# Optimization experiments

Hardware: AMD Instinct MI355X
Metric: run time of the kernel (lower is better)

The kernel has to match this reference:

```python
import jax, jax.numpy as jnp
import numpy as np

B, C, H, W = 2, 512, 64, 64
GROUPS = 32
EPS = 1e-6


def setup_inputs() -> dict:
    key = jax.random.key(0)
    ks = jax.random.split(key, 9)
    s = 1.0 / np.sqrt(C)
    return {
        "x": jax.random.normal(ks[0], (B, C, H, W), dtype=jnp.float32),
        "gamma": jnp.ones((C,), dtype=jnp.float32),
        "beta": jnp.zeros((C,), dtype=jnp.float32),
        "wq": jax.random.normal(ks[1], (C, C), dtype=jnp.float32) * s,
        "bq": jnp.zeros((C,), dtype=jnp.float32),
        "wk": jax.random.normal(ks[2], (C, C), dtype=jnp.float32) * s,
        "bk": jnp.zeros((C,), dtype=jnp.float32),
        "wv": jax.random.normal(ks[3], (C, C), dtype=jnp.float32) * s,
        "bv": jnp.zeros((C,), dtype=jnp.float32),
        "wp": jax.random.normal(ks[4], (C, C), dtype=jnp.float32) * s,
        "bp": jnp.zeros((C,), dtype=jnp.float32),
    }


def _group_norm(x, gamma, beta):
    b, c, h, w = x.shape
    xg = x.reshape(b, GROUPS, c // GROUPS, h, w)
    mean = jnp.mean(xg, axis=(2, 3, 4), keepdims=True)
    var = jnp.var(xg, axis=(2, 3, 4), keepdims=True)
    xn = ((xg - mean) * jax.lax.rsqrt(var + EPS)).reshape(b, c, h, w)
    return xn * gamma[None, :, None, None] + beta[None, :, None, None]


def reference(x, gamma, beta, wq, bq, wk, bk, wv, bv, wp, bp):
    b, c, h, w = x.shape
    hn = _group_norm(x, gamma, beta)
    # 1x1 convs == per-pixel linear; flatten spatial: (b, hw, c)
    t = hn.reshape(b, c, h * w).transpose(0, 2, 1)
    q = jnp.einsum('bnc,oc->bno', t, wq) + bq
    k = jnp.einsum('bnc,oc->bno', t, wk) + bk
    v = jnp.einsum('bnc,oc->bno', t, wv) + bv
    scale = float(int(c) ** (-0.5))
    attn = jax.nn.softmax(jnp.einsum('bic,bjc->bij', q, k) * scale, axis=-1)
    o = jnp.einsum('bij,bjc->bic', attn, v)  # (b, hw, c)
    o = jnp.einsum('bnc,oc->bno', o, wp) + bp
    o = o.transpose(0, 2, 1).reshape(b, c, h, w)
    return x + o
```

## Files before the change

kernel.cpp:

```cpp
#include <hip/hip_runtime.h>
#include <hip/hip_bf16.h>

#define B_ 2
#define C_ 512
#define HW_ 4096
#define K_ 512
#define EPS_ 1e-6f
#define SCALE_ 0.04419417382415922f
#define NEG_INF_ (-1e30f)

typedef __attribute__((ext_vector_type(8))) __bf16 bf16x8;
typedef __attribute__((ext_vector_type(4))) float f32x4;
typedef __attribute__((ext_vector_type(16))) float f32x16;

__device__ __forceinline__ unsigned short f2bf(float f) {
  union { float f; unsigned u; } v; v.f = f;
  unsigned r = v.u + 0x7fffu + ((v.u >> 16) & 1u);
  return (unsigned short)(r >> 16);
}
__device__ __forceinline__ float bf2f(unsigned short h) {
  union { unsigned u; float f; } v; v.u = ((unsigned)h) << 16;
  return v.f;
}

__device__ __forceinline__ void gld_lds16(const unsigned short* g, unsigned short* l) {
  __builtin_amdgcn_global_load_lds((const __attribute__((address_space(1))) void*)g,
                                   (__attribute__((address_space(3))) void*)l, 16, 0, 0);
}

__global__ void gn_sums(const float* __restrict__ x, float* __restrict__ stats) {
  int bid = blockIdx.x;
  int bg = bid >> 4, row = bid & 15;
  int b = bg >> 5, g = bg & 31;
  const float* base = x + ((size_t)(b * C_ + g * 16 + row)) * HW_;
  float s = 0.f, s2 = 0.f;
  int t = threadIdx.x;
  #pragma unroll
  for (int i = 0; i < 4; ++i) {
    float4 v = *reinterpret_cast<const float4*>(base + (size_t)(t + i * 256) * 4);
    s  += v.x + v.y + v.z + v.w;
    s2 += v.x * v.x + v.y * v.y + v.z * v.z + v.w * v.w;
  }
  for (int off = 32; off; off >>= 1) { s += __shfl_down(s, off); s2 += __shfl_down(s2, off); }
  __shared__ float rs[4], rs2[4];
  int w = t >> 6;
  if ((t & 63) == 0) { rs[w] = s; rs2[w] = s2; }
  __syncthreads();
  if (t == 0) {
    atomicAdd(&stats[bg], rs[0] + rs[1] + rs[2] + rs[3]);
    atomicAdd(&stats[64 + bg], rs2[0] + rs2[1] + rs2[2] + rs2[3]);
  }
}

__global__ void build_t(const float* __restrict__ x, const float* __restrict__ stats,
                        const float* __restrict__ gamma, const float* __restrict__ beta,
                        unsigned short* __restrict__ tb) {
  __shared__ float lds[64 * 69];
  int n0 = blockIdx.x * 64, c0 = blockIdx.y * 64, b = blockIdx.z;
  int t = threadIdx.x;
  {
    int cl = t >> 2, ch = t & 3;
    int c = c0 + cl;
    int bg = b * 32 + (c >> 4);
    float s = stats[bg], s2v = stats[64 + bg];
    float mean = s * (1.f / 65536.f);
    float var = s2v * (1.f / 65536.f) - mean * mean;
    float rstd = rsqrtf(var + EPS_);
    float ga = gamma[c] * rstd;
    float be = beta[c] - mean * ga;
    const float* xr = x + ((size_t)(b * C_ + c)) * HW_ + n0 + ch * 16;
    #pragma unroll
    for (int i = 0; i < 4; ++i) {
      float4 v = *reinterpret_cast<const float4*>(xr + i * 4);
      int nl = ch * 16 + i * 4;
      lds[cl * 69 + nl + 0] = v.x * ga + be;
      lds[cl * 69 + nl + 1] = v.y * ga + be;
      lds[cl * 69 + nl + 2] = v.z * ga + be;
      lds[cl * 69 + nl + 3] = v.w * ga + be;
    }
  }
  __syncthreads();
  {
    int nl = t >> 2, cw = t & 3;
    unsigned short* orow = tb + ((size_t)(b * HW_ + n0 + nl)) * C_ + c0 + cw * 16;
    #pragma unroll
    for (int i = 0; i < 4; ++i) {
      ushort4 o4;
      o4.x = f2bf(lds[(cw * 16 + i * 4 + 0) * 69 + nl]);
      o4.y = f2bf(lds[(cw * 16 + i * 4 + 1) * 69 + nl]);
      o4.z = f2bf(lds[(cw * 16 + i * 4 + 2) * 69 + nl]);
      o4.w = f2bf(lds[(cw * 16 + i * 4 + 3) * 69 + nl]);
      *reinterpret_cast<ushort4*>(orow + i * 4) = o4;
    }
  }
}

__global__ void cast_w4(const float* __restrict__ s0, const float* __restrict__ s1,
                        const float* __restrict__ s2, const float* __restrict__ s3,
                        unsigned short* __restrict__ dst) {
  int which = blockIdx.y;
  const float* src = which == 0 ? s0 : which == 1 ? s1 : which == 2 ? s2 : s3;
  int i = (blockIdx.x * 256 + threadIdx.x) * 4;
  float4 v = *reinterpret_cast<const float4*>(src + i);
  ushort4 o; o.x = f2bf(v.x); o.y = f2bf(v.y); o.z = f2bf(v.z); o.w = f2bf(v.w);
  *reinterpret_cast<ushort4*>(dst + (size_t)which * 262144 + i) = o;
}

__global__ __launch_bounds__(256, 2) void gemm_qkv(
    const unsigned short* __restrict__ tb, const unsigned short* __restrict__ wqkv,
    const float* __restrict__ bq, const float* __restrict__ bk, const float* __restrict__ bv,
    unsigned short* __restrict__ qb, unsigned short* __restrict__ kb,
    unsigned short* __restrict__ vTb) {
  __shared__ unsigned short Al[2][128 * 64];
  __shared__ unsigned short Bl[2][128 * 64];
  int z = blockIdx.z;
  int which = z >> 1, b = z & 1;
  const unsigned short* Ab = (which < 2) ? (tb + (size_t)b * HW_ * K_) : (wqkv + 2 * 262144);
  const unsigned short* Bb = (which < 2) ? (wqkv + which * 262144) : (tb + (size_t)b * HW_ * K_);
  int m0 = (which < 2) ? blockIdx.y * 128 : blockIdx.x * 128;
  int n0 = (which < 2) ? blockIdx.x * 128 : blockIdx.y * 128;
  int N = (which < 2) ? 512 : HW_;
  unsigned short* Cb = (which == 0) ? (qb + (size_t)b * HW_ * K_)
                     : (which == 1) ? (kb + (size_t)b * HW_ * K_)
                                    : (vTb + (size_t)b * C_ * HW_);
  const float* bias = (which == 0) ? bq : (which == 1) ? bk : bv;
  int t = threadIdx.x, lane = t & 63, w = t >> 6;
  int l15 = lane & 15, quad = lane >> 4;
  int mw = (w & 1) * 64, nw = (w >> 1) * 64;
  int sr8 = lane >> 3, sb = lane & 7;
  f32x4 acc[4][4] = {};

  #define G_STAGE(KC) do {                                                          \
    int pb = (KC) & 1;                                                              \
    _Pragma("unroll")                                                               \
    for (int q = 0; q < 4; ++q) {                                                   \
      int row = w * 32 + q * 8 + sr8;                                               \
      int gb = sb ^ (row & 7);                                                      \
      gld_lds16(Ab + (size_t)(m0 + row) * K_ + (KC) * 64 + gb * 8, &Al[pb][(w * 32 + q * 8) * 64]); \
      gld_lds16(Bb + (size_t)(n0 + row) * K_ + (KC) * 64 + gb * 8, &Bl[pb][(w * 32 + q * 8) * 64]); \
    }                                                                               \
  } while (0)

  G_STAGE(0);
  __syncthreads();
  for (int kc = 0; kc < 8; ++kc) {
    if (kc < 7) G_STAGE(kc + 1);
    const unsigned short* Ac = Al[kc & 1];
    const unsigned short* Bc = Bl[kc & 1];
    #pragma unroll
    for (int kk = 0; kk < 2; ++kk) {
      bf16x8 af[4];
      #pragma unroll
      for (int mt = 0; mt < 4; ++mt)
        af[mt] = *reinterpret_cast<const bf16x8*>(
            &Ac[(mw + mt * 16 + l15) * 64 + (((kk * 4 + quad) ^ (l15 & 7)) << 3)]);
      #pragma unroll
      for (int nt = 0; nt < 4; ++nt) {
        bf16x8 bfr = *reinterpret_cast<const bf16x8*>(
            &Bc[(nw + nt * 16 + l15) * 64 + (((kk * 4 + quad) ^ (l15 & 7)) << 3)]);
        #pragma unroll
        for (int mt = 0; mt < 4; ++mt)
          acc[mt][nt] = __builtin_amdgcn_mfma_f32_16x16x32_bf16(af[mt], bfr, acc[mt][nt], 0, 0, 0);
      }
    }
    __syncthreads();
  }
  #undef G_STAGE
  #pragma unroll
  for (int mt = 0; mt < 4; ++mt)
    #pragma unroll
    for (int nt = 0; nt < 4; ++nt)
      #pragma unroll
      for (int rr = 0; rr < 4; ++rr) {
        int row = m0 + mw + mt * 16 + quad * 4 + rr;
        int col = n0 + nw + nt * 16 + l15;
        float v = acc[mt][nt][rr] + ((which < 2) ? bias[col] : bias[row]);
        Cb[(size_t)row * N + col] = f2bf(v);
      }
}

template <int MODE>
__global__ __launch_bounds__(256, 2) void gemm_bt(
    const unsigned short* __restrict__ A, long sA,
    const unsigned short* __restrict__ B, long sB,
    void* __restrict__ Cv, long sC, int M, int N,
    const float* __restrict__ bias,
    const float* __restrict__ resid, long sR) {
  __shared__ unsigned short Al[2][128 * 64];
  __shared__ unsigned short Bl[2][128 * 64];
  int z = blockIdx.z;
  const unsigned short* Ab = A + (size_t)z * sA;
  const unsigned short* Bb = B + (size_t)z * sB;
  int n0 = blockIdx.x * 128, m0 = blockIdx.y * 128;
  int t = threadIdx.x, lane = t & 63, w = t >> 6;
  int l15 = lane & 15, quad = lane >> 4;
  int mw = (w & 1) * 64, nw = (w >> 1) * 64;
  int sr8 = lane >> 3, sb = lane & 7;
  f32x4 acc[4][4] = {};

  #define G_STAGE(KC) do {                                                          \
    int pb = (KC) & 1;                                                              \
    _Pragma("unroll")                                                               \
    for (int q = 0; q < 4; ++q) {                                                   \
      int row = w * 32 + q * 8 + sr8;                                               \
      int gb = sb ^ (row & 7);                                                      \
      gld_lds16(Ab + (size_t)(m0 + row) * K_ + (KC) * 64 + gb * 8, &Al[pb][(w * 32 + q * 8) * 64]); \
      gld_lds16(Bb + (size_t)(n0 + row) * K_ + (KC) * 64 + gb * 8, &Bl[pb][(w * 32 + q * 8) * 64]); \
    }                                                                               \
  } while (0)

  G_STAGE(0);
  __syncthreads();
  for (int kc = 0; kc < 8; ++kc) {
    if (kc < 7) G_STAGE(kc + 1);
    const unsigned short* Ac = Al[kc & 1];
    const unsigned short* Bc = Bl[kc & 1];
    #pragma unroll
    for (int kk = 0; kk < 2; ++kk) {
      bf16x8 af[4];
      #pragma unroll
      for (int mt = 0; mt < 4; ++mt)
        af[mt] = *reinterpret_cast<const bf16x8*>(
            &Ac[(mw + mt * 16 + l15) * 64 + (((kk * 4 + quad) ^ (l15 & 7)) << 3)]);
      #pragma unroll
      for (int nt = 0; nt < 4; ++nt) {
        bf16x8 bfr = *reinterpret_cast<const bf16x8*>(
            &Bc[(nw + nt * 16 + l15) * 64 + (((kk * 4 + quad) ^ (l15 & 7)) << 3)]);
        #pragma unroll
        for (int mt = 0; mt < 4; ++mt)
          acc[mt][nt] = __builtin_amdgcn_mfma_f32_16x16x32_bf16(af[mt], bfr, acc[mt][nt], 0, 0, 0);
      }
    }
    __syncthreads();
  }
  #undef G_STAGE
  #pragma unroll
  for (int mt = 0; mt < 4; ++mt)
    #pragma unroll
    for (int nt = 0; nt < 4; ++nt)
      #pragma unroll
      for (int rr = 0; rr < 4; ++rr) {
        int row = m0 + mw + mt * 16 + quad * 4 + rr;
        int col = n0 + nw + nt * 16 + l15;
        float v = acc[mt][nt][rr];
        if (MODE == 0) {
          v += bias[col];
          reinterpret_cast<unsigned short*>(Cv)[(size_t)z * sC + (size_t)row * N + col] = f2bf(v);
        } else if (MODE == 1) {
          v += bias[row];
          reinterpret_cast<unsigned short*>(Cv)[(size_t)z * sC + (size_t)row * N + col] = f2bf(v);
        } else {
          v += bias[row];
          v += resid[(size_t)z * sR + (size_t)row * N + col];
          reinterpret_cast<float*>(Cv)[(size_t)z * sC + (size_t)row * N + col] = v;
        }
      }
}

__global__ __launch_bounds__(512, 2) void attn(
    const unsigned short* __restrict__ qg, const unsigned short* __restrict__ kg,
    const unsigned short* __restrict__ vg,
    unsigned short* __restrict__ opart, float* __restrict__ mpart, float* __restrict__ lpart) {
  __shared__ unsigned short KVb[2 * 16384];
  __shared__ unsigned short Pl[64 * 264];
  __shared__ float sm_m[64], sm_l[64], sm_alpha[64], sm_red[128];
  int qt = blockIdx.x, jh = blockIdx.y, b = blockIdx.z;
  int t = threadIdx.x, lane = t & 63, w = t >> 6;
  int l15 = lane & 15, quad = lane >> 4;
  int l31 = lane & 31, hl = lane >> 5;
  int rw = w & 3, cw = w >> 2;
  int rw2 = w & 1, dg = w >> 1;
  int m0 = qt * 64;
  if (t < 64) { sm_m[t] = NEG_INF_; sm_l[t] = 0.f; }

  int st_r[4], st_kb[4];
  #pragma unroll
  for (int q = 0; q < 4; ++q) {
    int blk = w * 4 + q;
    st_r[q] = blk * 4 + (lane >> 4);
    st_kb[q] = (lane & 15) ^ (st_r[q] & 7);
  }

  #define STAGE_K(JC, KC, J0) do {                                                  \
    const unsigned short* gb = kg + ((size_t)(b * HW_ + (J0) + (JC) * 128)) * K_ + (KC) * 128; \
    unsigned short* lb = KVb + ((((JC) * 4 + (KC)) & 1) << 14);                     \
    _Pragma("unroll")                                                               \
    for (int q = 0; q < 4; ++q)                                                     \
      gld_lds16(gb + (size_t)st_r[q] * K_ + st_kb[q] * 8, lb + (w * 4 + q) * 512);  \
  } while (0)

  #define STAGE_V(DC, JC, J0) do {                                                 \
    const unsigned short* gb = vg + ((size_t)(b * K_ + (DC) * 128)) * HW_ + (J0) + (JC) * 128; \
    unsigned short* lb = KVb + (((DC) & 1) << 14);                                  \
    _Pragma("unroll")                                                               \
    for (int q = 0; q < 4; ++q)                                                     \
      gld_lds16(gb + (size_t)st_r[q] * HW_ + st_kb[q] * 8, lb + (w * 4 + q) * 512); \
  } while (0)

  bf16x8 qa[16];
  {
    const unsigned short* qrow = qg + ((size_t)(b * HW_ + m0 + rw * 16 + l15)) * K_ + quad * 8;
    #pragma unroll
    for (int kk = 0; kk < 16; ++kk)
      qa[kk] = *reinterpret_cast<const bf16x8*>(qrow + kk * 32);
  }
  f32x16 acc_o[4] = {};

  int j0 = jh * 2048;
  STAGE_K(0, 0, j0);
  __syncthreads();

  for (int it = 0; it < 8; ++it, j0 += 256) {
    f32x4 acc_s[8] = {};
    #pragma unroll
    for (int c = 0; c < 8; ++c) {
      int jc = c >> 2, kc = c & 3;
      if (c < 7) { STAGE_K((c + 1) >> 2, (c + 1) & 3, j0); }
      else       { STAGE_V(0, 0, j0); }
      const unsigned short* bufc = KVb + ((c & 1) << 14);
      #pragma unroll
      for (int kk = 0; kk < 4; ++kk)
        #pragma unroll
        for (int ct = 0; ct < 4; ++ct) {
          int jr = cw * 64 + ct * 16 + l15;
          bf16x8 bfr = *reinterpret_cast<const bf16x8*>(
              &bufc[jr * 128 + (((kk * 4 + quad) ^ (l15 & 7)) << 3)]);
          acc_s[jc * 4 + ct] = __builtin_amdgcn_mfma_f32_16x16x32_bf16(qa[kc * 4 + kk], bfr, acc_s[jc * 4 + ct], 0, 0, 0);
        }
      __syncthreads();
    }
    float mx[4];
    #pragma unroll
    for (int rr = 0; rr < 4; ++rr) {
      float m = NEG_INF_;
      #pragma unroll
      for (int s = 0; s < 8; ++s) {
        acc_s[s][rr] *= SCALE_;
        m = fmaxf(m, acc_s[s][rr]);
      }
      mx[rr] = m;
    }
    #pragma unroll
    for (int off = 1; off < 16; off <<= 1)
      #pragma unroll
      for (int rr = 0; rr < 4; ++rr)
        mx[rr] = fmaxf(mx[rr], __shfl_xor(mx[rr], off));
    if (l15 == 0)
      #pragma unroll
      for (int rr = 0; rr < 4; ++rr)
        sm_red[cw * 64 + rw * 16 + quad * 4 + rr] = mx[rr];
    __syncthreads();
    if (t < 64) {
      float mnew = fmaxf(sm_m[t], fmaxf(sm_red[t], sm_red[64 + t]));
      sm_alpha[t] = __expf(sm_m[t] - mnew);
      sm_m[t] = mnew;
    }
    __syncthreads();
    float sum[4] = {0.f, 0.f, 0.f, 0.f};
    #pragma unroll
    for (int s = 0; s < 8; ++s)
      #pragma unroll
      for (int rr = 0; rr < 4; ++rr) {
        int rowl = rw * 16 + quad * 4 + rr;
        float p = __expf(acc_s[s][rr] - sm_m[rowl]);
        sum[rr] += p;
        Pl[rowl * 264 + (s >> 2) * 128 + cw * 64 + (s & 3) * 16 + l15] = f2bf(p);
      }
    #pragma unroll
    for (int off = 1; off < 16; off <<= 1)
      #pragma unroll
      for (int rr = 0; rr < 4; ++rr)
        sum[rr] += __shfl_xor(sum[rr], off);
    if (l15 == 0)
      #pragma unroll
      for (int rr = 0; rr < 4; ++rr)
        sm_red[cw * 64 + rw * 16 + quad * 4 + rr] = sum[rr];
    __syncthreads();
    if (t < 64)
      sm_l[t] = sm_l[t] * sm_alpha[t] + sm_red[t] + sm_red[64 + t];
    #pragma unroll
    for (int r16 = 0; r16 < 16; ++r16) {
      int row = rw2 * 32 + (r16 & 3) + 8 * (r16 >> 2) + 4 * hl;
      float a = sm_alpha[row];
      #pragma unroll
      for (int dc = 0; dc < 4; ++dc)
        acc_o[dc][r16] *= a;
    }
    bf16x8 pa_r[8];
    #pragma unroll
    for (int c = 0; c < 8; ++c) {
      int jc = c >> 2, dc = c & 3;
      if ((c & 3) == 0) {
        #pragma unroll
        for (int ksx = 0; ksx < 8; ++ksx)
          pa_r[ksx] = *reinterpret_cast<const bf16x8*>(
              &Pl[(rw2 * 32 + l31) * 264 + jc * 128 + ksx * 16 + hl * 8]);
      }
      if (c < 7)          { STAGE_V((c + 1) & 3, (c + 1) >> 2, j0); }
      else if (it < 7)    { STAGE_K(0, 0, j0 + 256); }
      const unsigned short* bufc = KVb + ((c & 1) << 14);
      #pragma unroll
      for (int ksx = 0; ksx < 8; ++ksx) {
        bf16x8 vb = *reinterpret_cast<const bf16x8*>(
            &bufc[(dg * 32 + l31) * 128 + (((ksx * 2 + hl) ^ (l31 & 7)) << 3)]);
        acc_o[dc] = __builtin_amdgcn_mfma_f32_32x32x16_bf16(pa_r[ksx], vb, acc_o[dc], 0, 0, 0);
      }
      __syncthreads();
    }
  }
  #undef STAGE_K
  #undef STAGE_V
  int part = jh * 2 + b;
  unsigned short* ob = opart + ((size_t)part * HW_ + m0) * 512;
  #pragma unroll
  for (int dc = 0; dc < 4; ++dc) {
    int d = dc * 128 + dg * 32 + l31;
    #pragma unroll
    for (int r16 = 0; r16 < 16; ++r16) {
      int row = rw2 * 32 + (r16 & 3) + 8 * (r16 >> 2) + 4 * hl;
      ob[(size_t)row * 512 + d] = f2bf(acc_o[dc][r16]);
    }
  }
  if (t < 64) {
    mpart[(size_t)part * HW_ + m0 + t] = sm_m[t];
    lpart[(size_t)part * HW_ + m0 + t] = sm_l[t];
  }
}

__global__ void merge_o(const unsigned short* __restrict__ opart, const float* __restrict__ mpart,
                        const float* __restrict__ lpart, unsigned short* __restrict__ om) {
  int rg = blockIdx.x;
  int b = rg >> 12, n = rg & 4095;
  float m[2], l[2], M = NEG_INF_;
  #pragma unroll
  for (int p = 0; p < 2; ++p) {
    size_t r = (size_t)(p * 2 + b) * HW_ + n;
    m[p] = mpart[r]; l[p] = lpart[r];
    M = fmaxf(M, m[p]);
  }
  float wgt[2], L = 0.f;
  #pragma unroll
  for (int p = 0; p < 2; ++p) { wgt[p] = __expf(m[p] - M); L += l[p] * wgt[p]; }
  float inv = 1.f / L;
  unsigned short* orow = om + (size_t)rg * 512;
  for (int d = threadIdx.x; d < 512; d += 256) {
    float acc = 0.f;
    #pragma unroll
    for (int p = 0; p < 2; ++p)
      acc += bf2f(opart[((size_t)(p * 2 + b) * HW_ + n) * 512 + d]) * wgt[p];
    orow[d] = f2bf(acc * inv);
  }
}

extern "C" void kernel_launch(void* const* d_in, const int* in_sizes, int n_in,
                              void* d_out, int out_size, void* d_ws, size_t ws_size,
                              hipStream_t stream) {
  const float* x     = (const float*)d_in[0];
  const float* gamma = (const float*)d_in[1];
  const float* beta  = (const float*)d_in[2];
  const float* wq    = (const float*)d_in[3];
  const float* bq    = (const float*)d_in[4];
  const float* wk    = (const float*)d_in[5];
  const float* bk    = (const float*)d_in[6];
  const float* wv    = (const float*)d_in[7];
  const float* bv    = (const float*)d_in[8];
  const float* wp    = (const float*)d_in[9];
  const float* bp    = (const float*)d_in[10];
  float* out = (float*)d_out;

  char* ws = (char*)d_ws;
  size_t o = 0;
  float* stats          = (float*)(ws + o);          o += 1024;
  unsigned short* tb    = (unsigned short*)(ws + o); o += 8388608;
  unsigned short* qb    = (unsigned short*)(ws + o); o += 8388608;
  unsigned short* kb    = (unsigned short*)(ws + o); o += 8388608;
  unsigned short* vTb   = (unsigned short*)(ws + o); o += 8388608;
  unsigned short* wqb   = (unsigned short*)(ws + o); o += 524288;
  unsigned short* wkb   = (unsigned short*)(ws + o); o += 524288;
  unsigned short* wvb   = (unsigned short*)(ws + o); o += 524288;
  unsigned short* wpb   = (unsigned short*)(ws + o); o += 524288;
  unsigned short* opart = (unsigned short*)(ws + o); o += 16777216;
  float* mpart          = (float*)(ws + o);          o += 65536;
  float* lpart          = (float*)(ws + o);          o += 65536;
  unsigned short* om    = tb;

  hipMemsetAsync(stats, 0, 512, stream);
  gn_sums<<<1024, 256, 0, stream>>>(x, stats);
  build_t<<<dim3(64, 8, 2), 256, 0, stream>>>(x, stats, gamma, beta, tb);
  cast_w4<<<dim3(256, 4), 256, 0, stream>>>(wq, wk, wv, wp, wqb);
  gemm_qkv<<<dim3(4, 32, 6), 256, 0, stream>>>(tb, wqb, bq, bk, bv, qb, kb, vTb);
  attn<<<dim3(64, 2, 2), 512, 0, stream>>>(qb, kb, vTb, opart, mpart, lpart);
  merge_o<<<8192, 256, 0, stream>>>(opart, mpart, lpart, om);
  gemm_bt<2><<<dim3(32, 4, 2), 256, 0, stream>>>(wpb, 0, om, (long)HW_ * K_, out, (long)C_ * HW_, C_, HW_, bp, x, (long)C_ * HW_);
}
```

Before: 279.6 us.

## Triple-buffer K/V staging in attention with vmcnt-based waits and priority hints

The attention kernel's K/V LDS staging moves from two buffers to three, with loads issued two chunks ahead. The full __syncthreads calls are replaced by raw s_barrier plus an explicit vmcnt wait, so global-to-LDS copies stay in flight across MFMA phases. s_setprio is raised around MFMA blocks, and the softmax reduction barriers become lgkmcnt-only waits. merge_o is also vectorized to handle two bf16 values per thread. The larger LDS footprint may reduce occupancy, and the hand-tuned waitcnt and barrier logic risks races.

```diff
diff --git a/kernel.cpp b/kernel.cpp
--- a/kernel.cpp
+++ b/kernel.cpp
@@ -261,7 +261,7 @@
     const unsigned short* __restrict__ qg, const unsigned short* __restrict__ kg,
     const unsigned short* __restrict__ vg,
     unsigned short* __restrict__ opart, float* __restrict__ mpart, float* __restrict__ lpart) {
-  __shared__ unsigned short KVb[2 * 16384];
+  __shared__ unsigned short KVb[3 * 16384];
   __shared__ unsigned short Pl[64 * 264];
   __shared__ float sm_m[64], sm_l[64], sm_alpha[64], sm_red[128];
   int qt = blockIdx.x, jh = blockIdx.y, b = blockIdx.z;
@@ -281,20 +281,38 @@
     st_kb[q] = (lane & 15) ^ (st_r[q] & 7);
   }
 
-  #define STAGE_K(JC, KC, J0) do {                                                  \
-    const unsigned short* gb = kg + ((size_t)(b * HW_ + (J0) + (JC) * 128)) * K_ + (KC) * 128; \
-    unsigned short* lb = KVb + ((((JC) * 4 + (KC)) & 1) << 14);                     \
-    _Pragma("unroll")                                                               \
-    for (int q = 0; q < 4; ++q)                                                     \
-      gld_lds16(gb + (size_t)st_r[q] * K_ + st_kb[q] * 8, lb + (w * 4 + q) * 512);  \
+  #define STAGE_CH(Q, J0V, LB) do {                                                 \
+    if ((Q) < 8) {                                                                  \
+      const unsigned short* gb = kg + ((size_t)(b * HW_ + (J0V) + ((Q) >> 2) * 128)) * K_ + ((Q) & 3) * 128; \
+      _Pragma("unroll")                                                             \
+      for (int q_ = 0; q_ < 4; ++q_)                                                \
+        gld_lds16(gb + (size_t)st_r[q_] * K_ + st_kb[q_] * 8, (LB) + (w * 4 + q_) * 512); \
+    } else if ((Q) < 16) {                                                          \
+      const unsigned short* gb = vg + ((size_t)(b * K_ + (((Q) - 8) & 3) * 128)) * HW_ + (J0V) + (((Q) - 8) >> 2) * 128; \
+      _Pragma("unroll")                                                             \
+      for (int q_ = 0; q_ < 4; ++q_)                                                \
+        gld_lds16(gb + (size_t)st_r[q_] * HW_ + st_kb[q_] * 8, (LB) + (w * 4 + q_) * 512); \
+    } else {                                                                        \
+       \
+      const unsigned short* gb = kg + ((size_t)(b * HW_ + (J0V) + 256)) * K_ + ((Q) - 16) * 128; \
+      _Pragma("unroll")                                                             \
+      for (int q_ = 0; q_ < 4; ++q_)                                                \
+        gld_lds16(gb + (size_t)st_r[q_] * K_ + st_kb[q_] * 8, (LB) + (w * 4 + q_) * 512); \
+    }                                                                               \
   } while (0)
 
-  #define STAGE_V(DC, JC, J0) do {                                                 \
-    const unsigned short* gb = vg + ((size_t)(b * K_ + (DC) * 128)) * HW_ + (J0) + (JC) * 128; \
-    unsigned short* lb = KVb + (((DC) & 1) << 14);                                  \
-    _Pragma("unroll")                                                               \
-    for (int q = 0; q < 4; ++q)                                                     \
-      gld_lds16(gb + (size_t)st_r[q] * HW_ + st_kb[q] * 8, lb + (w * 4 + q) * 512); \
+  #define PHASE_PRE(Q) do {                                                         \
+    __builtin_amdgcn_s_barrier();                 \
+    int bs_ = bufr + 2; if (bs_ >= 3) bs_ -= 3;                                     \
+    STAGE_CH(Q, j0, KVb + bs_ * 16384);                                             \
+    asm volatile("s_waitcnt vmcnt(8)" ::: "memory");     \
+    __builtin_amdgcn_s_barrier();                  \
+    __builtin_amdgcn_sched_barrier(0);                                              \
+  } while (0)
+  #define PHASE_POST() do { bufr = (bufr + 1 >= 3) ? 0 : bufr + 1; } while (0)
+  #define LGKM_BAR() do {                                                           \
+    asm volatile("s_waitcnt lgkmcnt(0)" ::: "memory");                              \
+    __builtin_amdgcn_s_barrier();                                                   \
   } while (0)
 
   bf16x8 qa[16];
@@ -307,17 +325,18 @@
   f32x16 acc_o[4] = {};
 
   int j0 = jh * 2048;
-  STAGE_K(0, 0, j0);
-  __syncthreads();
+  int bufr = 0;
+  STAGE_CH(0, j0, KVb + 0 * 16384);
+  STAGE_CH(1, j0, KVb + 1 * 16384);
 
   for (int it = 0; it < 8; ++it, j0 += 256) {
     f32x4 acc_s[8] = {};
     #pragma unroll
     for (int c = 0; c < 8; ++c) {
-      int jc = c >> 2, kc = c & 3;
-      if (c < 7) { STAGE_K((c + 1) >> 2, (c + 1) & 3, j0); }
-      else       { STAGE_V(0, 0, j0); }
-      const unsigned short* bufc = KVb + ((c & 1) << 14);
+      PHASE_PRE(c + 2);
+      const unsigned short* bufc = KVb + bufr * 16384;
+      int jc = c >> 2;
+      __builtin_amdgcn_s_setprio(1);
       #pragma unroll
       for (int kk = 0; kk < 4; ++kk)
         #pragma unroll
@@ -325,9 +344,10 @@
           int jr = cw * 64 + ct * 16 + l15;
           bf16x8 bfr = *reinterpret_cast<const bf16x8*>(
               &bufc[jr * 128 + (((kk * 4 + quad) ^ (l15 & 7)) << 3)]);
-          acc_s[jc * 4 + ct] = __builtin_amdgcn_mfma_f32_16x16x32_bf16(qa[kc * 4 + kk], bfr, acc_s[jc * 4 + ct], 0, 0, 0);
+          acc_s[jc * 4 + ct] = __builtin_amdgcn_mfma_f32_16x16x32_bf16(qa[(c & 3) * 4 + kk], bfr, acc_s[jc * 4 + ct], 0, 0, 0);
         }
-      __syncthreads();
+      __builtin_amdgcn_s_setprio(0);
+      PHASE_POST();
     }
     float mx[4];
     #pragma unroll
@@ -349,13 +369,13 @@
       #pragma unroll
       for (int rr = 0; rr < 4; ++rr)
         sm_red[cw * 64 + rw * 16 + quad * 4 + rr] = mx[rr];
-    __syncthreads();
+    LGKM_BAR();
     if (t < 64) {
       float mnew = fmaxf(sm_m[t], fmaxf(sm_red[t], sm_red[64 + t]));
       sm_alpha[t] = __expf(sm_m[t] - mnew);
       sm_m[t] = mnew;
     }
-    __syncthreads();
+    LGKM_BAR();
     float sum[4] = {0.f, 0.f, 0.f, 0.f};
     #pragma unroll
     for (int s = 0; s < 8; ++s)
@@ -375,7 +395,7 @@
       #pragma unroll
       for (int rr = 0; rr < 4; ++rr)
         sm_red[cw * 64 + rw * 16 + quad * 4 + rr] = sum[rr];
-    __syncthreads();
+    LGKM_BAR();
     if (t < 64)
       sm_l[t] = sm_l[t] * sm_alpha[t] + sm_red[t] + sm_red[64 + t];
     #pragma unroll
@@ -389,6 +409,7 @@
     bf16x8 pa_r[8];
     #pragma unroll
     for (int c = 0; c < 8; ++c) {
+      PHASE_PRE(10 + c);
       int jc = c >> 2, dc = c & 3;
       if ((c & 3) == 0) {
         #pragma unroll
@@ -396,20 +417,22 @@
           pa_r[ksx] = *reinterpret_cast<const bf16x8*>(
               &Pl[(rw2 * 32 + l31) * 264 + jc * 128 + ksx * 16 + hl * 8]);
       }
-      if (c < 7)          { STAGE_V((c + 1) & 3, (c + 1) >> 2, j0); }
-      else if (it < 7)    { STAGE_K(0, 0, j0 + 256); }
-      const unsigned short* bufc = KVb + ((c & 1) << 14);
+      const unsigned short* bufc = KVb + bufr * 16384;
+      __builtin_amdgcn_s_setprio(1);
       #pragma unroll
       for (int ksx = 0; ksx < 8; ++ksx) {
         bf16x8 vb = *reinterpret_cast<const bf16x8*>(
             &bufc[(dg * 32 + l31) * 128 + (((ksx * 2 + hl) ^ (l31 & 7)) << 3)]);
         acc_o[dc] = __builtin_amdgcn_mfma_f32_32x32x16_bf16(pa_r[ksx], vb, acc_o[dc], 0, 0, 0);
       }
-      __syncthreads();
-    }
-  }
-  #undef STAGE_K
-  #undef STAGE_V
+      __builtin_amdgcn_s_setprio(0);
+      PHASE_POST();
+    }
+  }
+  #undef STAGE_CH
+  #undef PHASE_PRE
+  #undef PHASE_POST
+  #undef LGKM_BAR
   int part = jh * 2 + b;
   unsigned short* ob = opart + ((size_t)part * HW_ + m0) * 512;
   #pragma unroll
@@ -442,14 +465,17 @@
   #pragma unroll
   for (int p = 0; p < 2; ++p) { wgt[p] = __expf(m[p] - M); L += l[p] * wgt[p]; }
   float inv = 1.f / L;
-  unsigned short* orow = om + (size_t)rg * 512;
-  for (int d = threadIdx.x; d < 512; d += 256) {
-    float acc = 0.f;
-    #pragma unroll
-    for (int p = 0; p < 2; ++p)
-      acc += bf2f(opart[((size_t)(p * 2 + b) * HW_ + n) * 512 + d]) * wgt[p];
-    orow[d] = f2bf(acc * inv);
-  }
+  int d = threadIdx.x * 2;
+  float a0 = 0.f, a1 = 0.f;
+  #pragma unroll
+  for (int p = 0; p < 2; ++p) {
+    unsigned u = *reinterpret_cast<const unsigned*>(
+        &opart[((size_t)(p * 2 + b) * HW_ + n) * 512 + d]);
+    a0 += bf2f((unsigned short)(u & 0xffffu)) * wgt[p];
+    a1 += bf2f((unsigned short)(u >> 16)) * wgt[p];
+  }
+  unsigned out = (unsigned)f2bf(a0 * inv) | ((unsigned)f2bf(a1 * inv) << 16);
+  *reinterpret_cast<unsigned*>(om + (size_t)rg * 512 + d) = out;
 }
 
 extern "C" void kernel_launch(void* const* d_in, const int* in_sizes, int n_in,
```

Measured after the change: 278.4 us. About the same (-0.4%).

## Split attention KV range four ways with smaller LDS stages for higher occupancy

Applied to the files above, without the earlier changes.

The attention kernel now splits the key/value sequence into four partitions instead of two, so it launches 512 blocks instead of 256. The LDS staging buffers are halved to 64-column chunks so more blocks fit per CU, and launch bounds are raised to 4 blocks. The merge kernel combines four partials with vectorised 32-bit loads and stores. This trades more partial-output traffic and more pipeline stages with extra barriers for better CU fill on the MI355X.

```diff
diff --git a/kernel.cpp b/kernel.cpp
--- a/kernel.cpp
+++ b/kernel.cpp
@@ -257,11 +257,11 @@
       }
 }
 
-__global__ __launch_bounds__(512, 2) void attn(
+__global__ __launch_bounds__(512, 4) void attn(
     const unsigned short* __restrict__ qg, const unsigned short* __restrict__ kg,
     const unsigned short* __restrict__ vg,
     unsigned short* __restrict__ opart, float* __restrict__ mpart, float* __restrict__ lpart) {
-  __shared__ unsigned short KVb[2 * 16384];
+  __shared__ unsigned short KVb[2 * 8192];
   __shared__ unsigned short Pl[64 * 264];
   __shared__ float sm_m[64], sm_l[64], sm_alpha[64], sm_red[128];
   int qt = blockIdx.x, jh = blockIdx.y, b = blockIdx.z;
@@ -273,28 +273,29 @@
   int m0 = qt * 64;
   if (t < 64) { sm_m[t] = NEG_INF_; sm_l[t] = 0.f; }
 
-  int st_r[4], st_kb[4];
-  #pragma unroll
-  for (int q = 0; q < 4; ++q) {
-    int blk = w * 4 + q;
-    st_r[q] = blk * 4 + (lane >> 4);
-    st_kb[q] = (lane & 15) ^ (st_r[q] & 7);
-  }
-
-  #define STAGE_K(JC, KC, J0) do {                                                  \
-    const unsigned short* gb = kg + ((size_t)(b * HW_ + (J0) + (JC) * 128)) * K_ + (KC) * 128; \
-    unsigned short* lb = KVb + ((((JC) * 4 + (KC)) & 1) << 14);                     \
-    _Pragma("unroll")                                                               \
-    for (int q = 0; q < 4; ++q)                                                     \
-      gld_lds16(gb + (size_t)st_r[q] * K_ + st_kb[q] * 8, lb + (w * 4 + q) * 512);  \
-  } while (0)
-
-  #define STAGE_V(DC, JC, J0) do {                                                 \
-    const unsigned short* gb = vg + ((size_t)(b * K_ + (DC) * 128)) * HW_ + (J0) + (JC) * 128; \
-    unsigned short* lb = KVb + (((DC) & 1) << 14);                                  \
-    _Pragma("unroll")                                                               \
-    for (int q = 0; q < 4; ++q)                                                     \
-      gld_lds16(gb + (size_t)st_r[q] * HW_ + st_kb[q] * 8, lb + (w * 4 + q) * 512); \
+  #define STAGE_PH(P, J0V) do {                                                     \
+    unsigned short* lb = KVb + (((P) & 1) << 13);                                   \
+    if ((P) < 16 || (P) == 32) {                                                    \
+      int jcc = ((P) == 32) ? 0 : ((P) >> 3);                                       \
+      int jb = ((P) == 32) ? ((J0V) + 256) : (J0V);                                 \
+      int kcc = ((P) == 32) ? 0 : ((P) & 7);                                        \
+      _Pragma("unroll")                                                             \
+      for (int q_ = 0; q_ < 2; ++q_) {                                              \
+        int row = w * 16 + q_ * 8 + (lane >> 3);                                    \
+        int blk = (lane & 7) ^ (row & 7);                                           \
+        gld_lds16(kg + ((size_t)(b * HW_ + jb + jcc * 128 + row)) * K_ + kcc * 64 + blk * 8, \
+                  lb + (w * 16 + q_ * 8) * 64);                                     \
+      }                                                                             \
+    } else {                                                                        \
+      int jvv = ((P) - 16) >> 2, dcc = ((P) - 16) & 3;                              \
+      _Pragma("unroll")                                                             \
+      for (int q_ = 0; q_ < 2; ++q_) {                                              \
+        int row = w * 16 + q_ * 8 + (lane >> 3);                                    \
+        int blk = (lane & 7) ^ (row & 7);                                           \
+        gld_lds16(vg + ((size_t)(b * K_ + dcc * 128 + row)) * HW_ + (J0V) + jvv * 64 + blk * 8, \
+                  lb + (w * 16 + q_ * 8) * 64);                                     \
+      }                                                                             \
+    }                                                                               \
   } while (0)
 
   bf16x8 qa[16];
@@ -306,26 +307,26 @@
   }
   f32x16 acc_o[4] = {};
 
-  int j0 = jh * 2048;
-  STAGE_K(0, 0, j0);
+  int j0 = jh * 1024;
+  STAGE_PH(0, j0);
   __syncthreads();
 
-  for (int it = 0; it < 8; ++it, j0 += 256) {
+  for (int it = 0; it < 4; ++it, j0 += 256) {
     f32x4 acc_s[8] = {};
     #pragma unroll
-    for (int c = 0; c < 8; ++c) {
-      int jc = c >> 2, kc = c & 3;
-      if (c < 7) { STAGE_K((c + 1) >> 2, (c + 1) & 3, j0); }
-      else       { STAGE_V(0, 0, j0); }
-      const unsigned short* bufc = KVb + ((c & 1) << 14);
-      #pragma unroll
-      for (int kk = 0; kk < 4; ++kk)
+    for (int c = 0; c < 16; ++c) {
+      STAGE_PH(c + 1, j0);
+      const unsigned short* bufc = KVb + ((c & 1) << 13);
+      int jc = c >> 3, kc = c & 7;
+      #pragma unroll
+      for (int kk = 0; kk < 2; ++kk)
         #pragma unroll
         for (int ct = 0; ct < 4; ++ct) {
           int jr = cw * 64 + ct * 16 + l15;
           bf16x8 bfr = *reinterpret_cast<const bf16x8*>(
-              &bufc[jr * 128 + (((kk * 4 + quad) ^ (l15 & 7)) << 3)]);
-          acc_s[jc * 4 + ct] = __builtin_amdgcn_mfma_f32_16x16x32_bf16(qa[kc * 4 + kk], bfr, acc_s[jc * 4 + ct], 0, 0, 0);
+              &bufc[jr * 64 + (((kk * 4 + quad) ^ (jr & 7)) << 3)]);
+          acc_s[jc * 4 + ct] = __builtin_amdgcn_mfma_f32_16x16x32_bf16(
+              qa[kc * 2 + kk], bfr, acc_s[jc * 4 + ct], 0, 0, 0);
         }
       __syncthreads();
     }
@@ -386,30 +387,29 @@
       for (int dc = 0; dc < 4; ++dc)
         acc_o[dc][r16] *= a;
     }
-    bf16x8 pa_r[8];
-    #pragma unroll
-    for (int c = 0; c < 8; ++c) {
-      int jc = c >> 2, dc = c & 3;
+    bf16x8 pa_r[4];
+    #pragma unroll
+    for (int c = 0; c < 16; ++c) {
+      int jv = c >> 2, dc = c & 3;
       if ((c & 3) == 0) {
         #pragma unroll
-        for (int ksx = 0; ksx < 8; ++ksx)
+        for (int ksx = 0; ksx < 4; ++ksx)
           pa_r[ksx] = *reinterpret_cast<const bf16x8*>(
-              &Pl[(rw2 * 32 + l31) * 264 + jc * 128 + ksx * 16 + hl * 8]);
-      }
-      if (c < 7)          { STAGE_V((c + 1) & 3, (c + 1) >> 2, j0); }
-      else if (it < 7)    { STAGE_K(0, 0, j0 + 256); }
-      const unsigned short* bufc = KVb + ((c & 1) << 14);
-      #pragma unroll
-      for (int ksx = 0; ksx < 8; ++ksx) {
+              &Pl[(rw2 * 32 + l31) * 264 + jv * 64 + ksx * 16 + hl * 8]);
+      }
+      if (c < 15)       { STAGE_PH(17 + c, j0); }
+      else if (it < 3)  { STAGE_PH(32, j0); }
+      const unsigned short* bufc = KVb + (((16 + c) & 1) << 13);
+      #pragma unroll
+      for (int ksx = 0; ksx < 4; ++ksx) {
         bf16x8 vb = *reinterpret_cast<const bf16x8*>(
-            &bufc[(dg * 32 + l31) * 128 + (((ksx * 2 + hl) ^ (l31 & 7)) << 3)]);
+            &bufc[(dg * 32 + l31) * 64 + (((ksx * 2 + hl) ^ (l31 & 7)) << 3)]);
         acc_o[dc] = __builtin_amdgcn_mfma_f32_32x32x16_bf16(pa_r[ksx], vb, acc_o[dc], 0, 0, 0);
       }
       __syncthreads();
     }
   }
-  #undef STAGE_K
-  #undef STAGE_V
+  #undef STAGE_PH
   int part = jh * 2 + b;
   unsigned short* ob = opart + ((size_t)part * HW_ + m0) * 512;
   #pragma unroll
@@ -431,25 +431,28 @@
                         const float* __restrict__ lpart, unsigned short* __restrict__ om) {
   int rg = blockIdx.x;
   int b = rg >> 12, n = rg & 4095;
-  float m[2], l[2], M = NEG_INF_;
-  #pragma unroll
-  for (int p = 0; p < 2; ++p) {
+  float m[4], l[4], M = NEG_INF_;
+  #pragma unroll
+  for (int p = 0; p < 4; ++p) {
     size_t r = (size_t)(p * 2 + b) * HW_ + n;
     m[p] = mpart[r]; l[p] = lpart[r];
     M = fmaxf(M, m[p]);
   }
-  float wgt[2], L = 0.f;
-  #pragma unroll
-  for (int p = 0; p < 2; ++p) { wgt[p] = __expf(m[p] - M); L += l[p] * wgt[p]; }
+  float wgt[4], L = 0.f;
+  #pragma unroll
+  for (int p = 0; p < 4; ++p) { wgt[p] = __expf(m[p] - M); L += l[p] * wgt[p]; }
   float inv = 1.f / L;
-  unsigned short* orow = om + (size_t)rg * 512;
-  for (int d = threadIdx.x; d < 512; d += 256) {
-    float acc = 0.f;
-    #pragma unroll
-    for (int p = 0; p < 2; ++p)
-      acc += bf2f(opart[((size_t)(p * 2 + b) * HW_ + n) * 512 + d]) * wgt[p];
-    orow[d] = f2bf(acc * inv);
-  }
+  int d = threadIdx.x * 2;
+  float a0 = 0.f, a1 = 0.f;
+  #pragma unroll
+  for (int p = 0; p < 4; ++p) {
+    unsigned u = *reinterpret_cast<const unsigned*>(
+        &opart[((size_t)(p * 2 + b) * HW_ + n) * 512 + d]);
+    a0 += bf2f((unsigned short)(u & 0xffffu)) * wgt[p];
+    a1 += bf2f((unsigned short)(u >> 16)) * wgt[p];
+  }
+  unsigned out = (unsigned)f2bf(a0 * inv) | ((unsigned)f2bf(a1 * inv) << 16);
+  *reinterpret_cast<unsigned*>(om + (size_t)rg * 512 + d) = out;
 }
 
 extern "C" void kernel_launch(void* const* d_in, const int* in_sizes, int n_in,
@@ -479,9 +482,9 @@
   unsigned short* wkb   = (unsigned short*)(ws + o); o += 524288;
   unsigned short* wvb   = (unsigned short*)(ws + o); o += 524288;
   unsigned short* wpb   = (unsigned short*)(ws + o); o += 524288;
-  unsigned short* opart = (unsigned short*)(ws + o); o += 16777216;
-  float* mpart          = (float*)(ws + o);          o += 65536;
-  float* lpart          = (float*)(ws + o);          o += 65536;
+  unsigned short* opart = (unsigned short*)(ws + o); o += 33554432;
+  float* mpart          = (float*)(ws + o);          o += 131072;
+  float* lpart          = (float*)(ws + o);          o += 131072;
   unsigned short* om    = tb;
 
   hipMemsetAsync(stats, 0, 512, stream);
@@ -489,7 +492,7 @@
   build_t<<<dim3(64, 8, 2), 256, 0, stream>>>(x, stats, gamma, beta, tb);
   cast_w4<<<dim3(256, 4), 256, 0, stream>>>(wq, wk, wv, wp, wqb);
   gemm_qkv<<<dim3(4, 32, 6), 256, 0, stream>>>(tb, wqb, bq, bk, bv, qb, kb, vTb);
-  attn<<<dim3(64, 2, 2), 512, 0, stream>>>(qb, kb, vTb, opart, mpart, lpart);
+  attn<<<dim3(64, 4, 2), 512, 0, stream>>>(qb, kb, vTb, opart, mpart, lpart);
   merge_o<<<8192, 256, 0, stream>>>(opart, mpart, lpart, om);
   gemm_bt<2><<<dim3(32, 4, 2), 256, 0, stream>>>(wpb, 0, om, (long)HW_ * K_, out, (long)C_ * HW_, C_, HW_, bp, x, (long)C_ * HW_);
 }
```

Result: slower. 420.5 us (+50.4%).
